# Optimization experiments

Hardware: AMD Instinct MI355X
Metric: run time of the kernel (lower is better)

## Reference

```python
import jax, jax.numpy as jnp
import numpy as np

N, T, E, H, K = 16, 1024, 1024, 256, 3
MAX_OUT = 4 * T          # static upper bound on upsampled length (padded; torch uses dynamic max)
DUR_FACTOR = 1.0
MIN_DUR = 0
LN_EPS = 1e-5


def setup_inputs() -> dict:
    key = jax.random.key(0)
    ks = jax.random.split(key, 6)
    seqs = jax.random.normal(ks[0], (N, T, E), dtype=jnp.float32)
    lens = jax.random.randint(ks[1], (N,), T // 2, T + 1)
    padding_mask = jnp.arange(T)[None, :] < lens[:, None]  # True = valid frame
    s = 0.02
    return {
        "seqs": seqs,
        "conv1_w": jax.random.normal(ks[2], (H, E, K), jnp.float32) * s,
        "conv1_b": jnp.zeros((H,), jnp.float32),
        "ln1_g": jnp.ones((H,), jnp.float32),
        "ln1_b": jnp.zeros((H,), jnp.float32),
        "conv2_w": jax.random.normal(ks[3], (H, H, K), jnp.float32) * s,
        "conv2_b": jnp.zeros((H,), jnp.float32),
        "ln2_g": jnp.ones((H,), jnp.float32),
        "ln2_b": jnp.zeros((H,), jnp.float32),
        "proj_w": jax.random.normal(ks[4], (H,), jnp.float32) * s,
        "proj_b": jnp.float32(1.1),  # pushes mean duration to ~2 frames
        "padding_mask": padding_mask,
    }


def _conv1d(x, w, b):
    # x: [N, C_in, T], w: [C_out, C_in, K], 'same' padding for K=3
    y = jax.lax.conv_general_dilated(x, w, window_strides=(1,), padding=[(1, 1)],
                                     dimension_numbers=("NCH", "OIH", "NCH"))
    return y + b[None, :, None]


def _layernorm(x, g, b):
    mu = jnp.mean(x, axis=-1, keepdims=True)
    var = jnp.mean(jnp.square(x - mu), axis=-1, keepdims=True)
    return (x - mu) * jax.lax.rsqrt(var + LN_EPS) * g + b


def _variance_predictor(seqs, padding_mask, c1w, c1b, g1, b1, c2w, c2b, g2, b2, pw, pb):
    m = padding_mask[..., None].astype(seqs.dtype)  # [N, T, 1]
    x = seqs * m
    x = jax.nn.relu(_conv1d(x.transpose(0, 2, 1), c1w, c1b)).transpose(0, 2, 1)  # [N, T, H]
    x = _layernorm(x, g1, b1)
    # dropout in eval mode = identity
    x = x * m
    x = jax.nn.relu(_conv1d(x.transpose(0, 2, 1), c2w, c2b)).transpose(0, 2, 1)
    x = _layernorm(x, g2, b2)
    return jnp.einsum("nth,h->nt", x, pw) + pb  # log durations [N, T]


def reference(seqs, conv1_w, conv1_b, ln1_g, ln1_b, conv2_w, conv2_b, ln2_g, ln2_b,
              proj_w, proj_b, padding_mask):
    log_dur = _variance_predictor(seqs, padding_mask, conv1_w, conv1_b, ln1_g, ln1_b,
                                  conv2_w, conv2_b, ln2_g, ln2_b, proj_w, proj_b)
    dur = jnp.round((jnp.exp(log_dur) - 1.0) * DUR_FACTOR).astype(jnp.int32)
    dur = jnp.maximum(dur, MIN_DUR)
    dur = jnp.where(padding_mask, dur, 0)  # apply_padding_mask on integer durations

    # HardUpsampling: output position t takes source frame i = searchsorted(cumsum(dur), t, 'right')
    cum = jnp.cumsum(dur, axis=1)                 # [N, T]
    seq_lens = cum[:, -1]                         # [N]
    pos = jnp.arange(MAX_OUT, dtype=jnp.int32)    # [MAX_OUT]
    idx = jax.vmap(lambda c: jnp.searchsorted(c, pos, side="right"))(cum)  # [N, MAX_OUT]
    idx = jnp.clip(idx, 0, T - 1)
    up = jnp.take_along_axis(seqs, idx[:, :, None], axis=1)  # [N, MAX_OUT, E]
    valid = pos[None, :] < seq_lens[:, None]
    up = jnp.where(valid[:, :, None], up, 0.0)
    return up, seq_lens
```

## Files before the change

kernel.cpp:

```cpp
#include <hip/hip_runtime.h>

#define N_ 16
#define T_ 1024
#define E_ 1024
#define H_ 256
#define MAXOUT 4096
#define M_ (N_ * T_)
#define NJ 768
#define NJ16 48

typedef _Float16 half_t;
typedef __attribute__((ext_vector_type(8))) _Float16 f16x8;
typedef __attribute__((ext_vector_type(4))) _Float16 f16x4;
typedef __attribute__((ext_vector_type(4))) float f32x4;

constexpr size_t Y1_OFF  = 0;
constexpr size_t Y2_OFF  = 25165824;
constexpr size_t A0P_OFF = 50331648;
constexpr size_t A2P_OFF = 83886080;

constexpr size_t B1P_OFF  = 0;
constexpr size_t B2P_OFF  = 1572864;
constexpr size_t DUR_OFF  = 1966080;
constexpr size_t CUM_OFF  = 2031616;

__device__ __forceinline__ float mask_at(const unsigned char* __restrict__ raw, int i) {
    if (raw[1] == 1) return raw[i] ? 1.0f : 0.0f;
    return reinterpret_cast<const int*>(raw)[i] ? 1.0f : 0.0f;
}

__device__ __forceinline__ void gload_lds16(const void* g, void* l) {
    __builtin_amdgcn_global_load_lds(
        (const __attribute__((address_space(1))) unsigned int*)g,
        (__attribute__((address_space(3))) unsigned int*)l, 16, 0, 0);
}

__global__ __launch_bounds__(256) void prep_all_kernel(
    const float* __restrict__ X, const unsigned char* __restrict__ mraw,
    const float* __restrict__ w1, const float* __restrict__ w2,
    half_t* __restrict__ A0p, half_t* __restrict__ B1p, half_t* __restrict__ B2p) {
    const int bid = blockIdx.x;
    if (bid < 1024) {
        const int bm = bid;
        const int l = threadIdx.x & 63;
        const int bk4 = threadIdx.x >> 6;
        const int row = bm * 16 + (l & 15);
        const float mv = mask_at(mraw, row);
        const float* src = X + (size_t)row * E_ + ((l >> 4) * 8);
#pragma unroll
        for (int g = 0; g < 8; ++g) {
            const int bk = g * 4 + bk4;
            float4 v0 = *reinterpret_cast<const float4*>(src + bk * 32);
            float4 v1 = *reinterpret_cast<const float4*>(src + bk * 32 + 4);
            float v[8] = {v0.x, v0.y, v0.z, v0.w, v1.x, v1.y, v1.z, v1.w};
            f16x8 h8;
#pragma unroll
            for (int j = 0; j < 8; ++j) h8[j] = (half_t)(v[j] * mv);
            *reinterpret_cast<f16x8*>(A0p + ((size_t)(bm * 32 + bk) * 64 + l) * 8) = h8;
        }
    } else {
        const bool isW1 = (bid < 1024 + 384);
        const int c = (isW1 ? (bid - 1024) : (bid - 1408)) * 256 + threadIdx.x;
        const int EIN = isW1 ? E_ : H_;
        const float* w = isW1 ? w1 : w2;
        half_t* Bp = isW1 ? B1p : B2p;
        const int l = c & 63;
        const int t = c >> 6;
        const int bj = t % NJ16;
        const int bk = t / NJ16;
        const int j = bj * 16 + (l & 15);
        const int k = j >> 8;
        const int h = j & 255;
        const int e0 = bk * 32 + ((l >> 4) * 8);
        f16x8 h8;
#pragma unroll
        for (int jj = 0; jj < 8; ++jj)
            h8[jj] = (half_t)w[((size_t)h * EIN + e0 + jj) * 3 + k];
        *reinterpret_cast<f16x8*>(Bp + (size_t)c * 8) = h8;
    }
}

template <int NBK>
__global__ __launch_bounds__(256, 4) void gemm_f16_kernel(
    const half_t* __restrict__ Ap, const half_t* __restrict__ Bp,
    half_t* __restrict__ Y) {
    __shared__ __align__(16) half_t lds[2][2][4096];
    const int tid = threadIdx.x;
    const int l = tid & 63;
    const int wv = tid >> 6;
    const int wr = wv >> 1, wc = wv & 1;

    const int d = blockIdx.x;
    const int work = (d & 7) * 96 + (d >> 3);
    const int bjIdx = work % 6;
    const int bmIdx = work / 6;
    const int bm0 = bmIdx * 8;
    const int bj0 = bjIdx * 8;

    f32x4 acc[4][4] = {};

    auto stage = [&](int kb, int buf) {
#pragma unroll
        for (int s = 0; s < 2; ++s) {
            const int q = tid + 256 * s;
            const int blk = q >> 6;
            const int ql = q & 63;
            gload_lds16(Ap + (((size_t)(bm0 + blk) * NBK + kb) * 64 + ql) * 8,
                        &lds[buf][0][(size_t)q * 8]);
            gload_lds16(Bp + (((size_t)kb * NJ16 + bj0 + blk) * 64 + ql) * 8,
                        &lds[buf][1][(size_t)q * 8]);
        }
    };

    stage(0, 0);
    int cur = 0;
    for (int kb = 0; kb < NBK; ++kb) {
        __syncthreads();
        if (kb + 1 < NBK) stage(kb + 1, cur ^ 1);

        f16x8 bf[4];
#pragma unroll
        for (int nb = 0; nb < 4; ++nb)
            bf[nb] = *reinterpret_cast<const f16x8*>(&lds[cur][1][((wc * 4 + nb) * 64 + l) * 8]);

        __builtin_amdgcn_s_setprio(1);
#pragma unroll
        for (int mb = 0; mb < 4; ++mb) {
            f16x8 af = *reinterpret_cast<const f16x8*>(&lds[cur][0][((wr * 4 + mb) * 64 + l) * 8]);
#pragma unroll
            for (int nb = 0; nb < 4; ++nb)
                acc[mb][nb] = __builtin_amdgcn_mfma_f32_16x16x32_f16(af, bf[nb], acc[mb][nb], 0, 0, 0);
        }
        __builtin_amdgcn_s_setprio(0);
        cur ^= 1;
    }

    const int mrow0 = bmIdx * 128 + wr * 64;
    const int jcol0 = bjIdx * 128 + wc * 64;
#pragma unroll
    for (int mb = 0; mb < 4; ++mb)
#pragma unroll
        for (int nb = 0; nb < 4; ++nb) {
            const int j = jcol0 + nb * 16 + (l & 15);
            const int mbase = mrow0 + mb * 16 + (l >> 4) * 4;
#pragma unroll
            for (int r = 0; r < 4; ++r)
                Y[(size_t)(mbase + r) * NJ + j] = (half_t)acc[mb][nb][r];
        }
}

__global__ __launch_bounds__(256) void ln1_kernel(
    const half_t* __restrict__ Y1, const float* __restrict__ cb,
    const float* __restrict__ g, const float* __restrict__ b,
    const unsigned char* __restrict__ mraw,
    half_t* __restrict__ A2p) {
    __shared__ float xs[16][260];
    const int bm = blockIdx.x;
    const int wvv = threadIdx.x >> 6;
    const int lane = threadIdx.x & 63;
    const int h0 = lane * 4;
    const float4 cb4 = *reinterpret_cast<const float4*>(&cb[h0]);
    const float4 g4  = *reinterpret_cast<const float4*>(&g[h0]);
    const float4 b4  = *reinterpret_cast<const float4*>(&b[h0]);
#pragma unroll
    for (int i = 0; i < 4; ++i) {
        const int r = wvv * 4 + i;
        const int t = bm * 16 + r;
        f16x4 c4 = *reinterpret_cast<const f16x4*>(&Y1[(size_t)t * NJ + 256 + h0]);
        float v[4];
#pragma unroll
        for (int j = 0; j < 4; ++j) v[j] = (float)c4[j];
        if ((t & (T_ - 1)) != 0) {
            f16x4 l4 = *reinterpret_cast<const f16x4*>(&Y1[(size_t)(t - 1) * NJ + h0]);
#pragma unroll
            for (int j = 0; j < 4; ++j) v[j] += (float)l4[j];
        }
        if ((t & (T_ - 1)) != T_ - 1) {
            f16x4 r4 = *reinterpret_cast<const f16x4*>(&Y1[(size_t)(t + 1) * NJ + 512 + h0]);
#pragma unroll
            for (int j = 0; j < 4; ++j) v[j] += (float)r4[j];
        }
        v[0] = fmaxf(v[0] + cb4.x, 0.f); v[1] = fmaxf(v[1] + cb4.y, 0.f);
        v[2] = fmaxf(v[2] + cb4.z, 0.f); v[3] = fmaxf(v[3] + cb4.w, 0.f);
        float s  = v[0] + v[1] + v[2] + v[3];
        float ss = v[0]*v[0] + v[1]*v[1] + v[2]*v[2] + v[3]*v[3];
#pragma unroll
        for (int off = 1; off < 64; off <<= 1) {
            s  += __shfl_xor(s, off);
            ss += __shfl_xor(ss, off);
        }
        const float mu  = s * (1.0f / H_);
        const float var = ss * (1.0f / H_) - mu * mu;
        const float inv = 1.0f / sqrtf(var + 1e-5f);
        const float mv = mask_at(mraw, t);
        float4 o;
        o.x = ((v[0] - mu) * inv * g4.x + b4.x) * mv;
        o.y = ((v[1] - mu) * inv * g4.y + b4.y) * mv;
        o.z = ((v[2] - mu) * inv * g4.z + b4.z) * mv;
        o.w = ((v[3] - mu) * inv * g4.w + b4.w) * mv;
        *reinterpret_cast<float4*>(&xs[r][h0]) = o;
    }
    __syncthreads();
#pragma unroll
    for (int s2 = 0; s2 < 2; ++s2) {
        const int q = threadIdx.x + 256 * s2;
        const int l = q & 63;
        const int bk = q >> 6;
        const int rr = l & 15;
        const int hh = bk * 32 + ((l >> 4) * 8);
        f16x8 h8;
#pragma unroll
        for (int jj = 0; jj < 8; ++jj) h8[jj] = (half_t)xs[rr][hh + jj];
        *reinterpret_cast<f16x8*>(A2p + ((size_t)(bm * 8 + bk) * 64 + l) * 8) = h8;
    }
}

__global__ __launch_bounds__(256) void ln2_proj_dur_kernel(
    const half_t* __restrict__ Y2, const float* __restrict__ cb,
    const float* __restrict__ g, const float* __restrict__ b,
    const float* __restrict__ pw, const float* __restrict__ pb,
    const unsigned char* __restrict__ mraw, int* __restrict__ dur) {
    const int t = blockIdx.x * 4 + (threadIdx.x >> 6);
    const int lane = threadIdx.x & 63;
    const int h0 = lane * 4;

    f16x4 c4 = *reinterpret_cast<const f16x4*>(&Y2[(size_t)t * NJ + 256 + h0]);
    float v[4];
#pragma unroll
    for (int i = 0; i < 4; ++i) v[i] = (float)c4[i];
    if ((t & (T_ - 1)) != 0) {
        f16x4 l4 = *reinterpret_cast<const f16x4*>(&Y2[(size_t)(t - 1) * NJ + h0]);
#pragma unroll
        for (int i = 0; i < 4; ++i) v[i] += (float)l4[i];
    }
    if ((t & (T_ - 1)) != T_ - 1) {
        f16x4 r4 = *reinterpret_cast<const f16x4*>(&Y2[(size_t)(t + 1) * NJ + 512 + h0]);
#pragma unroll
        for (int i = 0; i < 4; ++i) v[i] += (float)r4[i];
    }
    float4 cb4 = *reinterpret_cast<const float4*>(&cb[h0]);
    v[0] = fmaxf(v[0] + cb4.x, 0.f); v[1] = fmaxf(v[1] + cb4.y, 0.f);
    v[2] = fmaxf(v[2] + cb4.z, 0.f); v[3] = fmaxf(v[3] + cb4.w, 0.f);

    float s = v[0] + v[1] + v[2] + v[3];
    float ss = v[0]*v[0] + v[1]*v[1] + v[2]*v[2] + v[3]*v[3];
#pragma unroll
    for (int off = 1; off < 64; off <<= 1) {
        s  += __shfl_xor(s, off);
        ss += __shfl_xor(ss, off);
    }
    const float mu  = s * (1.0f / H_);
    const float var = ss * (1.0f / H_) - mu * mu;
    const float inv = 1.0f / sqrtf(var + 1e-5f);

    float4 g4 = *reinterpret_cast<const float4*>(&g[h0]);
    float4 b4 = *reinterpret_cast<const float4*>(&b[h0]);
    float4 p4 = *reinterpret_cast<const float4*>(&pw[h0]);
    float c = ((v[0]-mu)*inv*g4.x + b4.x) * p4.x
            + ((v[1]-mu)*inv*g4.y + b4.y) * p4.y
            + ((v[2]-mu)*inv*g4.z + b4.z) * p4.z
            + ((v[3]-mu)*inv*g4.w + b4.w) * p4.w;
#pragma unroll
    for (int off = 1; off < 64; off <<= 1) c += __shfl_xor(c, off);

    if (lane == 0) {
        const float ld = c + pb[0];
        const float dv = rintf(expf(ld) - 1.0f);
        int di = (int)dv;
        if (di < 0) di = 0;
        if (mask_at(mraw, t) == 0.0f) di = 0;
        dur[t] = di;
    }
}

__global__ __launch_bounds__(1024) void cumsum_kernel(
    const int* __restrict__ dur, int* __restrict__ cum,
    float* __restrict__ seq_lens_out) {
    __shared__ int s[1024];
    const int n = blockIdx.x, t = threadIdx.x;
    s[t] = dur[n * T_ + t];
    __syncthreads();
    for (int off = 1; off < 1024; off <<= 1) {
        int v = (t >= off) ? s[t - off] : 0;
        __syncthreads();
        s[t] += v;
        __syncthreads();
    }
    cum[n * T_ + t] = s[t];
    if (t == T_ - 1) seq_lens_out[n] = (float)s[t];
}

__global__ __launch_bounds__(256) void upsample_kernel(
    const float* __restrict__ seqs, const int* __restrict__ cum,
    float* __restrict__ out) {
    const int wid = blockIdx.x * 4 + (threadIdx.x >> 6);
    const int n = wid >> 12;
    const int p = wid & (MAXOUT - 1);
    const int lane = threadIdx.x & 63;
    const int* c = cum + n * T_;
    const int slen = c[T_ - 1];
    int lo = 0, hi = T_;
    while (lo < hi) {
        int mid = (lo + hi) >> 1;
        if (c[mid] <= p) lo = mid + 1; else hi = mid;
    }
    const int idx = (lo < T_ - 1) ? lo : (T_ - 1);
    const bool valid = (p < slen);
    const f32x4* src = reinterpret_cast<const f32x4*>(seqs + ((size_t)(n * T_ + idx) * E_));
    f32x4* dst = reinterpret_cast<f32x4*>(out + (size_t)wid * E_);
#pragma unroll
    for (int i = 0; i < 4; ++i) {
        f32x4 v = {0.f, 0.f, 0.f, 0.f};
        if (valid) v = src[lane + 64 * i];
        __builtin_nontemporal_store(v, &dst[lane + 64 * i]);
    }
}

extern "C" void kernel_launch(void* const* d_in, const int* in_sizes, int n_in,
                              void* d_out, int out_size, void* d_ws, size_t ws_size,
                              hipStream_t stream) {
    const float* seqs = (const float*)d_in[0];
    const float* w1   = (const float*)d_in[1];
    const float* b1   = (const float*)d_in[2];
    const float* g1   = (const float*)d_in[3];
    const float* bb1  = (const float*)d_in[4];
    const float* w2   = (const float*)d_in[5];
    const float* b2   = (const float*)d_in[6];
    const float* g2   = (const float*)d_in[7];
    const float* bb2  = (const float*)d_in[8];
    const float* pw   = (const float*)d_in[9];
    const float* pb   = (const float*)d_in[10];
    const unsigned char* mraw = (const unsigned char*)d_in[11];

    char* wsb = (char*)d_ws;
    half_t* B1p = (half_t*)(wsb + B1P_OFF);
    half_t* B2p = (half_t*)(wsb + B2P_OFF);
    int* dur = (int*)(wsb + DUR_OFF);
    int* cum = (int*)(wsb + CUM_OFF);

    char* outb = (char*)d_out;
    half_t* Y1  = (half_t*)(outb + Y1_OFF);
    half_t* Y2  = (half_t*)(outb + Y2_OFF);
    half_t* A0p = (half_t*)(outb + A0P_OFF);
    half_t* A2p = (half_t*)(outb + A2P_OFF);

    float* out      = (float*)d_out;
    float* slen_out = out + (size_t)N_ * MAXOUT * E_;

    prep_all_kernel<<<1504, 256, 0, stream>>>(seqs, mraw, w1, w2, A0p, B1p, B2p);
    gemm_f16_kernel<32><<<768, 256, 0, stream>>>(A0p, B1p, Y1);
    ln1_kernel<<<M_ / 16, 256, 0, stream>>>(Y1, b1, g1, bb1, mraw, A2p);
    gemm_f16_kernel<8><<<768, 256, 0, stream>>>(A2p, B2p, Y2);
    ln2_proj_dur_kernel<<<M_ / 4, 256, 0, stream>>>(Y2, b2, g2, bb2, pw, pb, mraw, dur);
    cumsum_kernel<<<N_, 1024, 0, stream>>>(dur, cum, slen_out);
    upsample_kernel<<<(N_ * MAXOUT) / 4, 256, 0, stream>>>(seqs, cum, out);
}
```

Measured before the change: 134.7 us.

## Fuse fp32-to-fp16 input conversion and masking into first conv GEMM

Removes the separate pass that converted and masked the fp32 input into a packed fp16 A buffer. The first GEMM now loads fp32 rows straight from the input into registers one k-block ahead, masks and converts them, and writes them to LDS while B is staged asynchronously. This avoids writing and re-reading a 32 MB intermediate and saves a launch. In exchange, each of the 6 column-tile blocks sharing a row tile re-reads the fp32 A data, doubling A bytes per load, and the conversion adds VALU work and register pressure inside the MFMA loop.

```diff
diff --git a/kernel.cpp b/kernel.cpp
--- a/kernel.cpp
+++ b/kernel.cpp
@@ -16,8 +16,7 @@
 
 constexpr size_t Y1_OFF  = 0;
 constexpr size_t Y2_OFF  = 25165824;
-constexpr size_t A0P_OFF = 50331648;
-constexpr size_t A2P_OFF = 83886080;
+constexpr size_t A2P_OFF = 50331648;
 
 constexpr size_t B1P_OFF  = 0;
 constexpr size_t B2P_OFF  = 1572864;
@@ -35,49 +34,130 @@
         (__attribute__((address_space(3))) unsigned int*)l, 16, 0, 0);
 }
 
-__global__ __launch_bounds__(256) void prep_all_kernel(
-    const float* __restrict__ X, const unsigned char* __restrict__ mraw,
+__global__ __launch_bounds__(256) void prep_w_kernel(
     const float* __restrict__ w1, const float* __restrict__ w2,
-    half_t* __restrict__ A0p, half_t* __restrict__ B1p, half_t* __restrict__ B2p) {
+    half_t* __restrict__ B1p, half_t* __restrict__ B2p) {
     const int bid = blockIdx.x;
-    if (bid < 1024) {
-        const int bm = bid;
-        const int l = threadIdx.x & 63;
-        const int bk4 = threadIdx.x >> 6;
-        const int row = bm * 16 + (l & 15);
-        const float mv = mask_at(mraw, row);
-        const float* src = X + (size_t)row * E_ + ((l >> 4) * 8);
-#pragma unroll
-        for (int g = 0; g < 8; ++g) {
-            const int bk = g * 4 + bk4;
-            float4 v0 = *reinterpret_cast<const float4*>(src + bk * 32);
-            float4 v1 = *reinterpret_cast<const float4*>(src + bk * 32 + 4);
-            float v[8] = {v0.x, v0.y, v0.z, v0.w, v1.x, v1.y, v1.z, v1.w};
-            f16x8 h8;
-#pragma unroll
-            for (int j = 0; j < 8; ++j) h8[j] = (half_t)(v[j] * mv);
-            *reinterpret_cast<f16x8*>(A0p + ((size_t)(bm * 32 + bk) * 64 + l) * 8) = h8;
-        }
-    } else {
-        const bool isW1 = (bid < 1024 + 384);
-        const int c = (isW1 ? (bid - 1024) : (bid - 1408)) * 256 + threadIdx.x;
-        const int EIN = isW1 ? E_ : H_;
-        const float* w = isW1 ? w1 : w2;
-        half_t* Bp = isW1 ? B1p : B2p;
-        const int l = c & 63;
-        const int t = c >> 6;
-        const int bj = t % NJ16;
-        const int bk = t / NJ16;
-        const int j = bj * 16 + (l & 15);
-        const int k = j >> 8;
-        const int h = j & 255;
-        const int e0 = bk * 32 + ((l >> 4) * 8);
-        f16x8 h8;
-#pragma unroll
-        for (int jj = 0; jj < 8; ++jj)
-            h8[jj] = (half_t)w[((size_t)h * EIN + e0 + jj) * 3 + k];
-        *reinterpret_cast<f16x8*>(Bp + (size_t)c * 8) = h8;
-    }
+    const bool isW1 = (bid < 384);
+    const int c = (isW1 ? bid : bid - 384) * 256 + threadIdx.x;
+    const int EIN = isW1 ? E_ : H_;
+    const float* w = isW1 ? w1 : w2;
+    half_t* Bp = isW1 ? B1p : B2p;
+    const int l = c & 63;
+    const int t = c >> 6;
+    const int bj = t % NJ16;
+    const int bk = t / NJ16;
+    const int j = bj * 16 + (l & 15);
+    const int k = j >> 8;
+    const int h = j & 255;
+    const int e0 = bk * 32 + ((l >> 4) * 8);
+    f16x8 h8;
+#pragma unroll
+    for (int jj = 0; jj < 8; ++jj)
+        h8[jj] = (half_t)w[((size_t)h * EIN + e0 + jj) * 3 + k];
+    *reinterpret_cast<f16x8*>(Bp + (size_t)c * 8) = h8;
+}
+
+__global__ __launch_bounds__(256, 4) void gemm1_fused_kernel(
+    const float* __restrict__ seqs, const unsigned char* __restrict__ mraw,
+    const half_t* __restrict__ Bp, half_t* __restrict__ Y) {
+    constexpr int NBK = 32;
+    __shared__ __align__(16) half_t lds[2][2][4096];
+    const int tid = threadIdx.x;
+    const int l = tid & 63;
+    const int wv = tid >> 6;
+    const int wr = wv >> 1, wc = wv & 1;
+
+    const int d = blockIdx.x;
+    const int work = (d & 7) * 96 + (d >> 3);
+    const int bjIdx = work % 6;
+    const int bmIdx = work / 6;
+    const int bm0 = bmIdx * 8;
+    const int bj0 = bjIdx * 8;
+
+    f32x4 acc[4][4] = {};
+    f32x4 rA[4];
+
+    const int r1 = (bm0 + (tid >> 6)) * 16 + (tid & 15);
+    const int r2 = r1 + 64;
+    const int cbase = ((tid & 63) >> 4) * 8;
+    const float mv1 = mask_at(mraw, r1);
+    const float mv2 = mask_at(mraw, r2);
+    const float* pA1 = seqs + (size_t)r1 * E_ + cbase;
+    const float* pA2 = seqs + (size_t)r2 * E_ + cbase;
+
+    auto issueA = [&](int kb) {
+        rA[0] = *reinterpret_cast<const f32x4*>(pA1 + kb * 32);
+        rA[1] = *reinterpret_cast<const f32x4*>(pA1 + kb * 32 + 4);
+        rA[2] = *reinterpret_cast<const f32x4*>(pA2 + kb * 32);
+        rA[3] = *reinterpret_cast<const f32x4*>(pA2 + kb * 32 + 4);
+    };
+    auto writeA = [&](int buf) {
+        f16x8 h1, h2;
+#pragma unroll
+        for (int j = 0; j < 4; ++j) {
+            h1[j]     = (half_t)(rA[0][j] * mv1);
+            h1[4 + j] = (half_t)(rA[1][j] * mv1);
+            h2[j]     = (half_t)(rA[2][j] * mv2);
+            h2[4 + j] = (half_t)(rA[3][j] * mv2);
+        }
+        *reinterpret_cast<f16x8*>(&lds[buf][0][(size_t)tid * 8]) = h1;
+        *reinterpret_cast<f16x8*>(&lds[buf][0][(size_t)(tid + 256) * 8]) = h2;
+    };
+    auto stageB = [&](int kb, int buf) {
+#pragma unroll
+        for (int s = 0; s < 2; ++s) {
+            const int q = tid + 256 * s;
+            const int blk = q >> 6;
+            const int ql = q & 63;
+            gload_lds16(Bp + (((size_t)kb * NJ16 + bj0 + blk) * 64 + ql) * 8,
+                        &lds[buf][1][(size_t)q * 8]);
+        }
+    };
+
+    issueA(0);
+    stageB(0, 0);
+    writeA(0);
+
+    int cur = 0;
+    for (int kb = 0; kb < NBK; ++kb) {
+        __syncthreads();
+        if (kb + 1 < NBK) {
+            issueA(kb + 1);
+            stageB(kb + 1, cur ^ 1);
+        }
+
+        f16x8 bf[4];
+#pragma unroll
+        for (int nb = 0; nb < 4; ++nb)
+            bf[nb] = *reinterpret_cast<const f16x8*>(&lds[cur][1][((wc * 4 + nb) * 64 + l) * 8]);
+
+        __builtin_amdgcn_s_setprio(1);
+#pragma unroll
+        for (int mb = 0; mb < 4; ++mb) {
+            f16x8 af = *reinterpret_cast<const f16x8*>(&lds[cur][0][((wr * 4 + mb) * 64 + l) * 8]);
+#pragma unroll
+            for (int nb = 0; nb < 4; ++nb)
+                acc[mb][nb] = __builtin_amdgcn_mfma_f32_16x16x32_f16(af, bf[nb], acc[mb][nb], 0, 0, 0);
+        }
+        __builtin_amdgcn_s_setprio(0);
+
+        if (kb + 1 < NBK) writeA(cur ^ 1);
+        cur ^= 1;
+    }
+
+    const int mrow0 = bmIdx * 128 + wr * 64;
+    const int jcol0 = bjIdx * 128 + wc * 64;
+#pragma unroll
+    for (int mb = 0; mb < 4; ++mb)
+#pragma unroll
+        for (int nb = 0; nb < 4; ++nb) {
+            const int j = jcol0 + nb * 16 + (l & 15);
+            const int mbase = mrow0 + mb * 16 + (l >> 4) * 4;
+#pragma unroll
+            for (int r = 0; r < 4; ++r)
+                Y[(size_t)(mbase + r) * NJ + j] = (half_t)acc[mb][nb][r];
+        }
 }
 
 template <int NBK>
@@ -341,14 +421,13 @@
     char* outb = (char*)d_out;
     half_t* Y1  = (half_t*)(outb + Y1_OFF);
     half_t* Y2  = (half_t*)(outb + Y2_OFF);
-    half_t* A0p = (half_t*)(outb + A0P_OFF);
     half_t* A2p = (half_t*)(outb + A2P_OFF);
 
     float* out      = (float*)d_out;
     float* slen_out = out + (size_t)N_ * MAXOUT * E_;
 
-    prep_all_kernel<<<1504, 256, 0, stream>>>(seqs, mraw, w1, w2, A0p, B1p, B2p);
-    gemm_f16_kernel<32><<<768, 256, 0, stream>>>(A0p, B1p, Y1);
+    prep_w_kernel<<<480, 256, 0, stream>>>(w1, w2, B1p, B2p);
+    gemm1_fused_kernel<<<768, 256, 0, stream>>>(seqs, mraw, B1p, Y1);
     ln1_kernel<<<M_ / 16, 256, 0, stream>>>(Y1, b1, g1, bb1, mraw, A2p);
     gemm_f16_kernel<8><<<768, 256, 0, stream>>>(A2p, B2p, Y2);
     ln2_proj_dur_kernel<<<M_ / 4, 256, 0, stream>>>(Y2, b2, g2, bb2, pw, pb, mraw, dur);
```

After: 155.6 us. 15.5% more time.
